# Performance work log

Measured on AMD Instinct MI355X. Metric: run time of the kernel, lower is better.

The kernel has to match this reference:

```python
import jax, jax.numpy as jnp
import numpy as np
from jax import lax

V, H, B, S, T = 32000, 512, 32, 256, 16  # vocab, hidden, batch, src_len, keyword_len


def setup_inputs() -> dict:
    key = jax.random.key(0)
    ks = jax.random.split(key, 26)
    sc = 0.02
    def P(k, *shape):
        return jax.random.normal(k, shape, jnp.float32) * sc
    return {
        "theme": jax.random.randint(ks[0], (1, B), 0, V),
        "keyword": jax.random.randint(ks[1], (T, B), 0, V),
        "src": jax.random.randint(ks[2], (S, B), 0, V),
        "theme_tab": P(ks[3], V, H),
        "keyword_tab": P(ks[4], V, H),
        "src_tab": P(ks[5], V, H),
        # GRU params (PyTorch layout: W_ih/W_hh are (3H, H) stacked r,z,n)
        "Wih_f": P(ks[6], 3 * H, H), "Whh_f": P(ks[7], 3 * H, H),
        "bih_f": P(ks[8], 3 * H), "bhh_f": P(ks[9], 3 * H),
        "Wih_b": P(ks[10], 3 * H, H), "Whh_b": P(ks[11], 3 * H, H),
        "bih_b": P(ks[12], 3 * H), "bhh_b": P(ks[13], 3 * H),
        # Linear layers (PyTorch layout: W is (out, in))
        "Ww": P(ks[14], H, 2 * H), "bw": P(ks[15], H),      # enc_w_weight
        "Wt": P(ks[16], H, H), "bt": P(ks[17], H),          # enc_theme_weight
        "Wk": P(ks[18], H, H), "bk": P(ks[19], H),          # enc_keyword_weight
        "wv": P(ks[20], H), "bv": P(ks[21]),                # enc_weight (H -> 1)
        "Wo": P(ks[22], H, 3 * H), "bo": P(ks[23], H),      # enc_output_out
        "Who": P(ks[24], H, 2 * H),                         # enc_hidden_out (no bias)
    }


def _gru_dir(x, Wih, Whh, bih, bhh, reverse):
    # x: (S, B, H). Returns (outputs (S,B,H), final hidden (B,H)).
    h = Whh.shape[1]
    gx = jnp.einsum('sbh,gh->sbg', x, Wih) + bih  # precompute input gates for all steps
    if reverse:
        gx = gx[::-1]
    h0 = jnp.zeros((x.shape[1], h), x.dtype)

    def step(hprev, g):
        gh = hprev @ Whh.T + bhh
        xr, xz, xn = jnp.split(g, 3, axis=-1)
        hr, hz, hn = jnp.split(gh, 3, axis=-1)
        r = jax.nn.sigmoid(xr + hr)
        z = jax.nn.sigmoid(xz + hz)
        n = jnp.tanh(xn + r * hn)
        hnew = (1.0 - z) * n + z * hprev
        return hnew, hnew

    hT, ys = lax.scan(step, h0, gx)
    if reverse:
        ys = ys[::-1]
    return ys, hT


def _forward(theme, keyword, src,
             theme_tab, keyword_tab, src_tab,
             Wih_f, Whh_f, bih_f, bhh_f,
             Wih_b, Whh_b, bih_b, bhh_b,
             Ww, bw, Wt, bt, Wk, bk, wv, bv, Wo, bo, Who):
    hdim = Whh_f.shape[1]
    src_emb = src_tab[src]          # (S, B, H)
    theme_emb = theme_tab[theme]    # (1, B, H)
    keyword_emb = keyword_tab[keyword]  # (T, B, H)

    ys_f, hT_f = _gru_dir(src_emb, Wih_f, Whh_f, bih_f, bhh_f, reverse=False)
    ys_b, hT_b = _gru_dir(src_emb, Wih_b, Whh_b, bih_b, bhh_b, reverse=True)
    enc_output = jnp.concatenate([ys_f, ys_b], axis=-1)   # (S, B, 2H); == enc_w_1 (the split/cat is identity)
    enc_hidden = jnp.concatenate([hT_f, hT_b], axis=-1)[None]  # (1, B, 2H)

    enc_w_1 = enc_output.transpose(1, 0, 2)     # (B, S, 2H)
    enc_theme = theme_emb.transpose(1, 0, 2)    # (B, 1, H)
    enc_keyword = keyword_emb.transpose(1, 0, 2)  # (B, T, H)

    # point(): additive-attention broadcast scoring
    b1 = enc_w_1 @ Ww.T + bw                    # (B, S, H)
    theme_proj = enc_theme[:, 0, :] @ Wt.T + bt  # (B, H)  == b22
    b3 = enc_keyword @ Wk.T + bk                # (B, T, H)
    b4 = jnp.tanh(b1[:, :, None, :] + theme_proj[:, None, None, :] + b3[:, None, :, :])  # (B,S,T,H)
    scores = b4 @ wv + bv                        # (B, S, T)
    enc_w_2 = jnp.einsum('bst,bh->bsh', scores, theme_proj)  # bmm(scores, b22 broadcast over T)

    concat_enc_w = jnp.concatenate([enc_w_2, enc_w_1], axis=-1)  # (B, S, 3H)
    enc_out = (concat_enc_w @ Wo.T + bo).transpose(1, 0, 2)      # (S, B, H)
    enc_hidden_out = enc_hidden @ Who.T                          # (1, B, H)
    return enc_out, enc_hidden_out


def reference(theme, keyword, src,
              theme_tab, keyword_tab, src_tab,
              Wih_f, Whh_f, bih_f, bhh_f,
              Wih_b, Whh_b, bih_b, bhh_b,
              Ww, bw, Wt, bt, Wk, bk, wv, bv, Wo, bo, Who):
    return _forward(theme, keyword, src,
                    theme_tab, keyword_tab, src_tab,
                    Wih_f, Whh_f, bih_f, bhh_f,
                    Wih_b, Whh_b, bih_b, bhh_b,
                    Ww, bw, Wt, bt, Wk, bk, wv, bv, Wo, bo, Who)
```

## Files before the change

### kernel.cpp

```cpp
#include <hip/hip_runtime.h>

typedef unsigned short u16;
typedef unsigned long long u64;
typedef __attribute__((ext_vector_type(8))) short bf16x8;
typedef __attribute__((ext_vector_type(4))) float f32x4;

__device__ __forceinline__ float bf2f(u16 u) {
  union { unsigned int i; float f; } v; v.i = ((unsigned int)u) << 16; return v.f;
}
__device__ __forceinline__ u16 f2bf(float f) {
  union { float f; unsigned int i; } v; v.f = f;
  unsigned int r = (v.i + 0x7FFFu + ((v.i >> 16) & 1u)) >> 16;
  return (u16)r;
}
__device__ __forceinline__ float sigmoidf_(float x) { return 1.f / (1.f + __expf(-x)); }
__device__ __forceinline__ float tanhf_(float x) {
  x = fminf(fmaxf(x, -10.f), 10.f);
  float e2 = __expf(2.f * x);
  return (e2 - 1.f) / (e2 + 1.f);
}

static const size_t OFF_GX    = 0;
static const size_t OFF_HBUF  = 50331648;
static const size_t OFF_ASRC  = 67174400;
static const size_t OFF_EW1   = 75563008;
static const size_t OFF_B1    = 92340224;
static const size_t OFF_WIHC  = 109117440;
static const size_t OFF_WWB   = 112263168;
static const size_t OFF_WO2B  = 113311744;
static const size_t OFF_WKB   = 114360320;
static const size_t OFF_KWE   = 114884608;
static const size_t OFF_B3    = 115408896;
static const size_t OFF_TP    = 116457472;
static const size_t OFF_TPO   = 116523008;
static const size_t OFF_SSUM  = 116588544;
static const size_t OFF_BIASC = 116621312;
static const size_t OFF_FLG   = 116633600;
static const size_t OFF_CLM   = OFF_FLG + 526336;

__global__ __launch_bounds__(256) void cvtk(const float* __restrict__ s,
                                            u16* __restrict__ d, int n) {
  int i = (blockIdx.x * 256 + threadIdx.x) * 4;
  if (i < n) {
    float4 v = *(const float4*)(s + i);
    ushort4 o; o.x = f2bf(v.x); o.y = f2bf(v.y); o.z = f2bf(v.z); o.w = f2bf(v.w);
    *(ushort4*)(d + i) = o;
  }
}

__global__ __launch_bounds__(256) void cvt_wo2(const float* __restrict__ Wo,
                                               u16* __restrict__ d) {
  int i = (blockIdx.x * 256 + threadIdx.x) * 4;
  int nrow = i >> 10, c = i & 1023;
  float4 v = *(const float4*)(Wo + (size_t)nrow * 1536 + 512 + c);
  ushort4 o; o.x = f2bf(v.x); o.y = f2bf(v.y); o.z = f2bf(v.z); o.w = f2bf(v.w);
  *(ushort4*)(d + i) = o;
}

__global__ __launch_bounds__(256) void gather_rows(const int* __restrict__ ids,
                                                   const float* __restrict__ tab,
                                                   u16* __restrict__ dst, int mode) {
  int i = (blockIdx.x * 256 + threadIdx.x) * 8;
  int r = i >> 9, c = i & 511;
  int id = (mode == 0) ? ids[r] : ids[((r & 15) << 5) + (r >> 4)];
  const float* s = tab + (size_t)id * 512 + c;
  alignas(16) u16 o[8];
#pragma unroll
  for (int j = 0; j < 8; ++j) o[j] = f2bf(s[j]);
  *(uint4*)(dst + i) = *(const uint4*)o;
}

__global__ __launch_bounds__(256) void proj_tp(const int* __restrict__ theme,
                                               const float* __restrict__ tab,
                                               const float* __restrict__ W,
                                               const float* __restrict__ bias,
                                               float* __restrict__ outp) {
  int o = blockIdx.x * 256 + threadIdx.x;
  int b = o >> 9, n = o & 511;
  const float* emb = tab + (size_t)theme[b] * 512;
  const float* wr = W + (size_t)n * 512;
  float acc = 0.f;
  for (int h = 0; h < 512; h += 4) {
    float4 e = *(const float4*)(emb + h);
    float4 w = *(const float4*)(wr + h);
    acc += e.x * w.x + e.y * w.y + e.z * w.z + e.w * w.w;
  }
  outp[o] = acc + bias[n];
}

__global__ __launch_bounds__(256) void proj_tpo(const float* __restrict__ tp,
                                                const float* __restrict__ Wo,
                                                float* __restrict__ outp) {
  int o = blockIdx.x * 256 + threadIdx.x;
  int b = o >> 9, n = o & 511;
  const float* emb = tp + (size_t)b * 512;
  const float* wr = Wo + (size_t)n * 1536;
  float acc = 0.f;
  for (int h = 0; h < 512; h += 4) {
    float4 e = *(const float4*)(emb + h);
    float4 w = *(const float4*)(wr + h);
    acc += e.x * w.x + e.y * w.y + e.z * w.z + e.w * w.w;
  }
  outp[o] = acc;
}

template <int EPI>
__global__ __launch_bounds__(256) void gemm_bt(const u16* __restrict__ A,
                                               const u16* __restrict__ B,
                                               const float* __restrict__ bias,
                                               float* __restrict__ Cf,
                                               u16* __restrict__ Cb, int M, int N,
                                               int K, const float* __restrict__ ssum,
                                               const float* __restrict__ tpo) {
  __shared__ u16 As[128][72];
  __shared__ u16 Bs[128][72];
  const int tid = threadIdx.x;
  const int mtiles = M >> 7;
  const int mt = blockIdx.x % mtiles, nt = blockIdx.x / mtiles;
  const int wave = tid >> 6, lane = tid & 63;
  const int wr = wave >> 1, wc = wave & 1;
  const int l16 = lane & 15, l4 = lane >> 4;
  f32x4 acc[4][4] = {};
  const int nkt = K >> 6;
  for (int kt = 0; kt < nkt; ++kt) {
    __syncthreads();
#pragma unroll
    for (int i = 0; i < 4; ++i) {
      int c = i * 256 + tid;
      int row = c >> 3, c8 = c & 7;
      uint4 va = *(const uint4*)(A + (size_t)(mt * 128 + row) * K + kt * 64 + c8 * 8);
      *(uint4*)&As[row][c8 * 8] = va;
      uint4 vb = *(const uint4*)(B + (size_t)(nt * 128 + row) * K + kt * 64 + c8 * 8);
      *(uint4*)&Bs[row][c8 * 8] = vb;
    }
    __syncthreads();
#pragma unroll
    for (int kk = 0; kk < 2; ++kk) {
      bf16x8 af[4], bfr[4];
#pragma unroll
      for (int m = 0; m < 4; ++m)
        af[m] = *(const bf16x8*)&As[wr * 64 + m * 16 + l16][kk * 32 + l4 * 8];
#pragma unroll
      for (int n = 0; n < 4; ++n)
        bfr[n] = *(const bf16x8*)&Bs[wc * 64 + n * 16 + l16][kk * 32 + l4 * 8];
#pragma unroll
      for (int m = 0; m < 4; ++m)
#pragma unroll
        for (int n = 0; n < 4; ++n)
          acc[m][n] = __builtin_amdgcn_mfma_f32_16x16x32_bf16(af[m], bfr[n],
                                                              acc[m][n], 0, 0, 0);
    }
  }
#pragma unroll
  for (int m = 0; m < 4; ++m) {
    int rg = mt * 128 + wr * 64 + m * 16 + l4 * 4;
#pragma unroll
    for (int n = 0; n < 4; ++n) {
      int cg = nt * 128 + wc * 64 + n * 16 + l16;
      float bb = bias[cg];
#pragma unroll
      for (int i = 0; i < 4; ++i) {
        int r = rg + i;
        float v = acc[m][n][i] + bb;
        if (EPI == 2) v += ssum[r] * tpo[(r & 31) * 512 + cg];
        if (EPI == 0) Cb[(size_t)r * N + cg] = f2bf(v);
        else Cf[(size_t)r * N + cg] = v;
      }
    }
  }
}

__global__ __launch_bounds__(512, 1) void gru_scan(
    const u16* __restrict__ gx,
    const float* __restrict__ Whh_f, const float* __restrict__ Whh_b,
    const float* __restrict__ bhh_f, const float* __restrict__ bhh_b,
    u16* __restrict__ hbuf,
    int* __restrict__ flg,
    int* __restrict__ clm)
{
  __shared__ float pbuf[4][3][4][64];
  __shared__ int sInfo[2];
  const int tid = threadIdx.x;

  int xcc;
  asm volatile("s_getreg_b32 %0, hwreg(HW_REG_XCC_ID)" : "=s"(xcc));
  xcc &= 7;
  if (tid == 0) {
    int r = __hip_atomic_fetch_add(&clm[xcc], 1, __ATOMIC_RELAXED,
                                   __HIP_MEMORY_SCOPE_AGENT);
    sInfo[0] = r;
    if (r == 31) {
      int exp = 0;
      __hip_atomic_compare_exchange_strong(&clm[8], &exp, xcc + 1,
                                           __ATOMIC_RELAXED, __ATOMIC_RELAXED,
                                           __HIP_MEMORY_SCOPE_AGENT);
    }
    int c;
    do {
      c = __hip_atomic_load(&clm[8], __ATOMIC_RELAXED, __HIP_MEMORY_SCOPE_AGENT);
      if (c == 0) __builtin_amdgcn_s_sleep(8);
    } while (c == 0);
    sInfo[1] = c - 1;
  }
  __syncthreads();
  const int rank = sInfo[0];
  if (sInfo[1] != xcc || rank >= 32) return;

  const int d = rank & 1;
  const int slice = rank >> 1;
  const float* Whh = d ? Whh_b : Whh_f;
  const float* bhh = d ? bhh_b : bhh_f;

  const int wave = tid >> 6, lane = tid & 63;
  const int kh = wave >> 2, m = (wave >> 1) & 1, a = wave & 1;
  const int p = m * 2 + a;
  const int l16 = lane & 15, l4 = lane >> 4;
  const int j = a * 16 + l16;

  bf16x8 wfrag[3][8];
#pragma unroll
  for (int g = 0; g < 3; ++g) {
    const float* wrow = Whh + (size_t)(g * 512 + slice * 32 + j) * 512;
#pragma unroll
    for (int kk = 0; kk < 8; ++kk) {
      const float* wp = wrow + (kh * 8 + kk) * 32 + l4 * 8;
      float4 v0 = *(const float4*)wp;
      float4 v1 = *(const float4*)(wp + 4);
      alignas(16) u16 tmp[8];
      tmp[0] = f2bf(v0.x); tmp[1] = f2bf(v0.y); tmp[2] = f2bf(v0.z); tmp[3] = f2bf(v0.w);
      tmp[4] = f2bf(v1.x); tmp[5] = f2bf(v1.y); tmp[6] = f2bf(v1.z); tmp[7] = f2bf(v1.w);
      wfrag[g][kk] = *(const bf16x8*)tmp;
    }
  }
  float bR = 0.f, bZ = 0.f, bN = 0.f;
  if (kh == 0) {
    bR = bhh[slice * 32 + j];
    bZ = bhh[512 + slice * 32 + j];
    bN = bhh[1024 + slice * 32 + j];
  }
  float hreg[4] = {0.f, 0.f, 0.f, 0.f};

  const size_t dbase = (size_t)d * 257 * 32 * 512;
  int* const flgd = flg + (size_t)d * 257 * 16 * 16;

  for (int t = 0; t < 256; ++t) {
    float xg[3][4];
    if (kh == 0) {
      int trow = d ? (255 - t) : t;
      const u16* gb = gx + (size_t)(trow * 32 + m * 16 + l4 * 4) * 3072 +
                      d * 1536 + slice * 32 + j;
#pragma unroll
      for (int i = 0; i < 4; ++i)
#pragma unroll
        for (int g = 0; g < 3; ++g)
          xg[g][i] = bf2f(gb[(size_t)i * 3072 + g * 512]);
      __builtin_amdgcn_sched_barrier(0);
    }

    if (t > 0) {
      if (wave == 4) {
        const int* fp = flgd + ((size_t)t * 16 + l16) * 16;
        while (true) {
          int v = __hip_atomic_load(fp, __ATOMIC_RELAXED, __HIP_MEMORY_SCOPE_AGENT);
          if (__all(v != 0)) break;
        }
      }
      __builtin_amdgcn_fence(__ATOMIC_ACQUIRE, "workgroup");
      __syncthreads();
    }

    const u16* hsrc = hbuf + dbase + (size_t)t * 32 * 512 +
                      (size_t)(m * 16 + l16) * 512 + kh * 256 + l4 * 8;
    uint4 areg[8];
#pragma unroll
    for (int kk = 0; kk < 8; ++kk)
      areg[kk] = *(const uint4*)(hsrc + kk * 32);

    f32x4 acc[3] = {};
#pragma unroll
    for (int kk = 0; kk < 8; ++kk) {
      union { uint4 u; bf16x8 v; } cv;
      cv.u = areg[kk];
#pragma unroll
      for (int g = 0; g < 3; ++g)
        acc[g] = __builtin_amdgcn_mfma_f32_16x16x32_bf16(cv.v, wfrag[g][kk],
                                                         acc[g], 0, 0, 0);
    }

    if (kh == 1) {
#pragma unroll
      for (int g = 0; g < 3; ++g)
#pragma unroll
        for (int i = 0; i < 4; ++i) pbuf[p][g][i][lane] = acc[g][i];
    }
    __syncthreads();

    if (kh == 0) {
      u16* hrow = hbuf + dbase + (size_t)(t + 1) * 32 * 512 + slice * 32;
#pragma unroll
      for (int i = 0; i < 4; ++i) {
        float hr = acc[0][i] + pbuf[p][0][i][lane] + bR;
        float hz = acc[1][i] + pbuf[p][1][i][lane] + bZ;
        float hn = acc[2][i] + pbuf[p][2][i][lane] + bN;
        float rr = sigmoidf_(xg[0][i] + hr);
        float zz = sigmoidf_(xg[1][i] + hz);
        float nn = tanhf_(xg[2][i] + rr * hn);
        hreg[i] = (1.f - zz) * nn + zz * hreg[i];
      }
#pragma unroll
      for (int i = 0; i < 4; ++i) {
        unsigned int myb = f2bf(hreg[i]);
        unsigned int ob = (unsigned int)__shfl_xor((int)myb, 1);
        if ((l16 & 1) == 0) {
          unsigned int w = (myb & 0xffffu) | (ob << 16);
          unsigned int* dst = (unsigned int*)(hrow +
                              (size_t)(m * 16 + l4 * 4 + i) * 512 + j);
          __hip_atomic_store(dst, w, __ATOMIC_RELAXED, __HIP_MEMORY_SCOPE_AGENT);
        }
      }
    }
    asm volatile("s_waitcnt vmcnt(0)" ::: "memory");
    __syncthreads();
    if (tid == 0)
      __hip_atomic_store(flgd + ((size_t)(t + 1) * 16 + slice) * 16, 1,
                         __ATOMIC_RELAXED, __HIP_MEMORY_SCOPE_AGENT);
  }
}

__global__ __launch_bounds__(256) void build_encw1(const u16* __restrict__ hbuf,
                                                   u16* __restrict__ ew) {
  int idx = (blockIdx.x * 256 + threadIdx.x) * 8;
  int r = idx >> 10, c = idx & 1023;
  int s = r >> 5, b = r & 31;
  size_t src;
  if (c < 512) src = ((size_t)(s + 1) * 32 + b) * 512 + c;
  else src = ((size_t)(257 + 256 - s) * 32 + b) * 512 + (c - 512);
  *(uint4*)(ew + idx) = *(const uint4*)(hbuf + src);
}

__global__ __launch_bounds__(256) void scores_k(const float* __restrict__ b1,
                                                const float* __restrict__ tp,
                                                const float* __restrict__ b3,
                                                const float* __restrict__ wv,
                                                const float* __restrict__ bv,
                                                float* __restrict__ ssum) {
  __shared__ float pre[512];
  __shared__ float wvs[512];
  __shared__ float red[4];
  int r = blockIdx.x;
  int tid = threadIdx.x;
  int b = r & 31;
  for (int h = tid; h < 512; h += 256) {
    pre[h] = b1[(size_t)r * 512 + h] + tp[b * 512 + h];
    wvs[h] = wv[h];
  }
  __syncthreads();
  float acc = 0.f;
  for (int t = 0; t < 16; ++t) {
    const float* b3r = b3 + ((size_t)b * 16 + t) * 512;
    for (int h = tid; h < 512; h += 256) acc += wvs[h] * tanhf_(pre[h] + b3r[h]);
  }
  for (int o = 32; o > 0; o >>= 1) acc += __shfl_down(acc, o);
  if ((tid & 63) == 0) red[tid >> 6] = acc;
  __syncthreads();
  if (tid == 0) ssum[r] = red[0] + red[1] + red[2] + red[3] + 16.f * bv[0];
}

__global__ __launch_bounds__(256) void hidden_k(const u16* __restrict__ hbuf,
                                                const float* __restrict__ Who,
                                                float* __restrict__ outp) {
  int o = blockIdx.x * 256 + threadIdx.x;
  int b = o >> 9, n = o & 511;
  const u16* hf = hbuf + ((size_t)256 * 32 + b) * 512;
  const u16* hb = hbuf + ((size_t)(257 + 256) * 32 + b) * 512;
  const float* w = Who + (size_t)n * 1024;
  float acc = 0.f;
  for (int k = 0; k < 512; ++k) acc += bf2f(hf[k]) * w[k];
  for (int k = 0; k < 512; ++k) acc += bf2f(hb[k]) * w[512 + k];
  outp[o] = acc;
}

extern "C" void kernel_launch(void* const* d_in, const int* in_sizes, int n_in,
                              void* d_out, int out_size, void* d_ws, size_t ws_size,
                              hipStream_t stream) {
  (void)in_sizes; (void)n_in; (void)out_size; (void)ws_size;
  const int* theme = (const int*)d_in[0];
  const int* keyword = (const int*)d_in[1];
  const int* src = (const int*)d_in[2];
  const float* theme_tab = (const float*)d_in[3];
  const float* keyword_tab = (const float*)d_in[4];
  const float* src_tab = (const float*)d_in[5];
  const float* Wih_f = (const float*)d_in[6];
  const float* Whh_f = (const float*)d_in[7];
  const float* bih_f = (const float*)d_in[8];
  const float* bhh_f = (const float*)d_in[9];
  const float* Wih_b = (const float*)d_in[10];
  const float* Whh_b = (const float*)d_in[11];
  const float* bih_b = (const float*)d_in[12];
  const float* bhh_b = (const float*)d_in[13];
  const float* Ww = (const float*)d_in[14];
  const float* bw = (const float*)d_in[15];
  const float* Wt = (const float*)d_in[16];
  const float* bt = (const float*)d_in[17];
  const float* Wk = (const float*)d_in[18];
  const float* bk = (const float*)d_in[19];
  const float* wv = (const float*)d_in[20];
  const float* bv = (const float*)d_in[21];
  const float* Wo = (const float*)d_in[22];
  const float* bo = (const float*)d_in[23];
  const float* Who = (const float*)d_in[24];
  float* out = (float*)d_out;
  char* ws = (char*)d_ws;

  u16* gx_cat = (u16*)(ws + OFF_GX);
  u16* hbuf = (u16*)(ws + OFF_HBUF);
  u16* asrc = (u16*)(ws + OFF_ASRC);
  u16* ew1 = (u16*)(ws + OFF_EW1);
  float* b1buf = (float*)(ws + OFF_B1);
  u16* wihc = (u16*)(ws + OFF_WIHC);
  u16* wwb = (u16*)(ws + OFF_WWB);
  u16* wo2b = (u16*)(ws + OFF_WO2B);
  u16* wkb = (u16*)(ws + OFF_WKB);
  u16* kwe = (u16*)(ws + OFF_KWE);
  float* b3buf = (float*)(ws + OFF_B3);
  float* tp = (float*)(ws + OFF_TP);
  float* tpo = (float*)(ws + OFF_TPO);
  float* ssum = (float*)(ws + OFF_SSUM);
  float* biasc = (float*)(ws + OFF_BIASC);
  int* flg = (int*)(ws + OFF_FLG);
  int* clm = (int*)(ws + OFF_CLM);

  hipMemsetAsync(flg, 0, 526336 + 64, stream);
  hipMemsetAsync(hbuf, 0, 32 * 512 * 2, stream);
  hipMemsetAsync(hbuf + (size_t)257 * 32 * 512, 0, 32 * 512 * 2, stream);
  hipMemcpyAsync(biasc, bih_f, 1536 * 4, hipMemcpyDeviceToDevice, stream);
  hipMemcpyAsync(biasc + 1536, bih_b, 1536 * 4, hipMemcpyDeviceToDevice, stream);

  cvtk<<<768, 256, 0, stream>>>(Wih_f, wihc, 1536 * 512);
  cvtk<<<768, 256, 0, stream>>>(Wih_b, wihc + 1536 * 512, 1536 * 512);
  cvtk<<<512, 256, 0, stream>>>(Ww, wwb, 512 * 1024);
  cvtk<<<256, 256, 0, stream>>>(Wk, wkb, 512 * 512);
  cvt_wo2<<<512, 256, 0, stream>>>(Wo, wo2b);
  gather_rows<<<2048, 256, 0, stream>>>(src, src_tab, asrc, 0);
  gather_rows<<<128, 256, 0, stream>>>(keyword, keyword_tab, kwe, 1);
  proj_tp<<<64, 256, 0, stream>>>(theme, theme_tab, Wt, bt, tp);
  proj_tpo<<<64, 256, 0, stream>>>(tp, Wo, tpo);
  gemm_bt<1><<<16, 256, 0, stream>>>(kwe, wkb, bk, b3buf, nullptr, 512, 512, 512,
                                     nullptr, nullptr);
  gemm_bt<0><<<1536, 256, 0, stream>>>(asrc, wihc, biasc, nullptr, gx_cat, 8192,
                                       3072, 512, nullptr, nullptr);
  gru_scan<<<256, 512, 0, stream>>>(gx_cat, Whh_f, Whh_b, bhh_f, bhh_b, hbuf, flg,
                                    clm);
  build_encw1<<<4096, 256, 0, stream>>>(hbuf, ew1);
  gemm_bt<1><<<256, 256, 0, stream>>>(ew1, wwb, bw, b1buf, nullptr, 8192, 512, 1024,
                                      nullptr, nullptr);
  scores_k<<<8192, 256, 0, stream>>>(b1buf, tp, b3buf, wv, bv, ssum);
  gemm_bt<2><<<256, 256, 0, stream>>>(ew1, wo2b, bo, out, nullptr, 8192, 512, 1024,
                                      ssum, tpo);
  hidden_k<<<64, 256, 0, stream>>>(hbuf, Who, out + 4194304);
}
```

Baseline: 1.293 ms.

## Use per-wave completion flags in GRU scan and prefetch next-step gates

The GRU recurrence kernel now publishes one readiness flag per wave (64 flags per step) right after each wave's stores, instead of a block-wide barrier followed by a single flag from thread 0. This removes one __syncthreads from each of the 256 sequential steps. The input-gate loads for step t+1 are issued after the flag store, so their latency overlaps the wait for other blocks. Separately, the b1 projection GEMM now writes bf16 instead of fp32 to halve that buffer's traffic into scores_k, at some precision cost.

```diff
diff --git a/kernel.cpp b/kernel.cpp
--- a/kernel.cpp
+++ b/kernel.cpp
@@ -241,25 +241,23 @@
   float hreg[4] = {0.f, 0.f, 0.f, 0.f};
 
   const size_t dbase = (size_t)d * 257 * 32 * 512;
-  int* const flgd = flg + (size_t)d * 257 * 16 * 16;
+  int* const flgd = flg + (size_t)d * 257 * 64 * 4;
+
+  u16 xgu[3][4];
+  if (kh == 0) {
+    const u16* gb = gx + (size_t)((d ? 255 : 0) * 32 + m * 16 + l4 * 4) * 3072 +
+                    d * 1536 + slice * 32 + j;
+#pragma unroll
+    for (int i = 0; i < 4; ++i)
+#pragma unroll
+      for (int g = 0; g < 3; ++g)
+        xgu[g][i] = gb[(size_t)i * 3072 + g * 512];
+  }
 
   for (int t = 0; t < 256; ++t) {
-    float xg[3][4];
-    if (kh == 0) {
-      int trow = d ? (255 - t) : t;
-      const u16* gb = gx + (size_t)(trow * 32 + m * 16 + l4 * 4) * 3072 +
-                      d * 1536 + slice * 32 + j;
-#pragma unroll
-      for (int i = 0; i < 4; ++i)
-#pragma unroll
-        for (int g = 0; g < 3; ++g)
-          xg[g][i] = bf2f(gb[(size_t)i * 3072 + g * 512]);
-      __builtin_amdgcn_sched_barrier(0);
-    }
-
     if (t > 0) {
       if (wave == 4) {
-        const int* fp = flgd + ((size_t)t * 16 + l16) * 16;
+        const int* fp = flgd + ((size_t)t * 64 + lane) * 4;
         while (true) {
           int v = __hip_atomic_load(fp, __ATOMIC_RELAXED, __HIP_MEMORY_SCOPE_AGENT);
           if (__all(v != 0)) break;
@@ -302,9 +300,9 @@
         float hr = acc[0][i] + pbuf[p][0][i][lane] + bR;
         float hz = acc[1][i] + pbuf[p][1][i][lane] + bZ;
         float hn = acc[2][i] + pbuf[p][2][i][lane] + bN;
-        float rr = sigmoidf_(xg[0][i] + hr);
-        float zz = sigmoidf_(xg[1][i] + hz);
-        float nn = tanhf_(xg[2][i] + rr * hn);
+        float rr = sigmoidf_(bf2f(xgu[0][i]) + hr);
+        float zz = sigmoidf_(bf2f(xgu[1][i]) + hz);
+        float nn = tanhf_(bf2f(xgu[2][i]) + rr * hn);
         hreg[i] = (1.f - zz) * nn + zz * hreg[i];
       }
 #pragma unroll
@@ -318,12 +316,21 @@
           __hip_atomic_store(dst, w, __ATOMIC_RELAXED, __HIP_MEMORY_SCOPE_AGENT);
         }
       }
-    }
-    asm volatile("s_waitcnt vmcnt(0)" ::: "memory");
-    __syncthreads();
-    if (tid == 0)
-      __hip_atomic_store(flgd + ((size_t)(t + 1) * 16 + slice) * 16, 1,
-                         __ATOMIC_RELAXED, __HIP_MEMORY_SCOPE_AGENT);
+      asm volatile("s_waitcnt vmcnt(0)" ::: "memory");
+      if (lane == 0)
+        __hip_atomic_store(flgd + ((size_t)(t + 1) * 64 + slice * 4 + p) * 4, 1,
+                           __ATOMIC_RELAXED, __HIP_MEMORY_SCOPE_AGENT);
+      if (t + 1 < 256) {
+        int trow = d ? (255 - (t + 1)) : (t + 1);
+        const u16* gb = gx + (size_t)(trow * 32 + m * 16 + l4 * 4) * 3072 +
+                        d * 1536 + slice * 32 + j;
+#pragma unroll
+        for (int i = 0; i < 4; ++i)
+#pragma unroll
+          for (int g = 0; g < 3; ++g)
+            xgu[g][i] = gb[(size_t)i * 3072 + g * 512];
+      }
+    }
   }
 }
 
@@ -338,7 +345,7 @@
   *(uint4*)(ew + idx) = *(const uint4*)(hbuf + src);
 }
 
-__global__ __launch_bounds__(256) void scores_k(const float* __restrict__ b1,
+__global__ __launch_bounds__(256) void scores_k(const u16* __restrict__ b1,
                                                 const float* __restrict__ tp,
                                                 const float* __restrict__ b3,
                                                 const float* __restrict__ wv,
@@ -351,7 +358,7 @@
   int tid = threadIdx.x;
   int b = r & 31;
   for (int h = tid; h < 512; h += 256) {
-    pre[h] = b1[(size_t)r * 512 + h] + tp[b * 512 + h];
+    pre[h] = bf2f(b1[(size_t)r * 512 + h]) + tp[b * 512 + h];
     wvs[h] = wv[h];
   }
   __syncthreads();
@@ -416,7 +423,7 @@
   u16* hbuf = (u16*)(ws + OFF_HBUF);
   u16* asrc = (u16*)(ws + OFF_ASRC);
   u16* ew1 = (u16*)(ws + OFF_EW1);
-  float* b1buf = (float*)(ws + OFF_B1);
+  u16* b1buf = (u16*)(ws + OFF_B1);
   u16* wihc = (u16*)(ws + OFF_WIHC);
   u16* wwb = (u16*)(ws + OFF_WWB);
   u16* wo2b = (u16*)(ws + OFF_WO2B);
@@ -445,14 +452,14 @@
   gather_rows<<<128, 256, 0, stream>>>(keyword, keyword_tab, kwe, 1);
   proj_tp<<<64, 256, 0, stream>>>(theme, theme_tab, Wt, bt, tp);
   proj_tpo<<<64, 256, 0, stream>>>(tp, Wo, tpo);
-  gemm_bt<1><<<16, 256, 0, stream>>>(kwe, wkb, bk, b3buf, nullptr, 512, 512, 512,
-                                     nullptr, nullptr);
+  gemm_bt<1><<<16, 256, 0, stream>>>(kwe, wkb, bk, (float*)(ws + OFF_B3), nullptr,
+                                     512, 512, 512, nullptr, nullptr);
   gemm_bt<0><<<1536, 256, 0, stream>>>(asrc, wihc, biasc, nullptr, gx_cat, 8192,
                                        3072, 512, nullptr, nullptr);
   gru_scan<<<256, 512, 0, stream>>>(gx_cat, Whh_f, Whh_b, bhh_f, bhh_b, hbuf, flg,
                                     clm);
   build_encw1<<<4096, 256, 0, stream>>>(hbuf, ew1);
-  gemm_bt<1><<<256, 256, 0, stream>>>(ew1, wwb, bw, b1buf, nullptr, 8192, 512, 1024,
+  gemm_bt<0><<<256, 256, 0, stream>>>(ew1, wwb, bw, nullptr, b1buf, 8192, 512, 1024,
                                       nullptr, nullptr);
   scores_k<<<8192, 256, 0, stream>>>(b1buf, tp, b3buf, wv, bv, ssum);
   gemm_bt<2><<<256, 256, 0, stream>>>(ew1, wo2b, bo, out, nullptr, 8192, 512, 1024,
```

After: 1.483 ms. 1.15x slower.
